# Kernel optimization log

Hardware: AMD Instinct MI355X
Metric: run time of the kernel (lower is better)

Reference implementation:

```python
import jax, jax.numpy as jnp
import numpy as np

N_NODES = 50000
N_EDGES = 1600000
DIM_IN = 64
DIM = 64
DIM_OUT = 32
N_GRAPHS = 64
DELTA = 2.5749
BN_EPS = 1e-5


def _lin(x, W, b):
    return x @ W.T + b


def _pna_conv(x, src, dst, mlp_W, mlp_b, W1, b1, W2, b2):
    # GINConv with overridden PNA aggregate: nn(x + aggr(x_j))
    msgs = x[src]                                               # [E, d]
    n = x.shape[0]
    sums = jax.ops.segment_sum(msgs, dst, num_segments=n)       # [N, d]
    maxs = jax.ops.segment_max(msgs, dst, num_segments=n)
    cnt = jax.ops.segment_sum(jnp.ones((msgs.shape[0], 1), msgs.dtype), dst,
                              num_segments=n)                   # [N, 1]
    means = sums / cnt
    var = jax.nn.relu(jax.ops.segment_sum(msgs * msgs, dst, num_segments=n) / cnt
                      - means * means)
    aggr = jnp.concatenate([sums, maxs, means, var], axis=1)    # [N, 4d]
    comb = jnp.concatenate([aggr, (cnt / DELTA) * aggr, (DELTA / cnt) * aggr],
                           axis=1)                              # [N, 12d]
    a = _lin(comb, mlp_W, mlp_b)                                # [N, d]
    h = x + a                                                   # (1+eps)*x + aggr, eps=0
    return _lin(jax.nn.relu(_lin(h, W1, b1)), W2, b2)


def _bn(x, g, b):
    # BatchNorm1d with batch statistics (training-mode stats, biased var)
    m = x.mean(axis=0)
    v = ((x - m) ** 2).mean(axis=0)
    return g * (x - m) / jnp.sqrt(v + BN_EPS) + b


def setup_inputs() -> dict:
    key = jax.random.key(0)
    ks = jax.random.split(key, 32)
    x = jax.random.normal(ks[0], (N_NODES, DIM_IN), dtype=jnp.float32)
    src = jax.random.randint(ks[1], (N_EDGES,), 0, N_NODES)
    dst = jax.random.randint(ks[2], (N_EDGES,), 0, N_NODES)
    # guarantee every node has >=1 incoming edge (original divides by bincount)
    dst = dst.at[:N_NODES].set(jnp.arange(N_NODES))
    edge_index = jnp.stack([src, dst]).astype(jnp.int32)
    batch = jnp.sort(jax.random.randint(ks[3], (N_NODES,), 0, N_GRAPHS)).astype(jnp.int32)

    def w(k, shape):
        return jax.random.normal(k, shape, dtype=jnp.float32) * 0.1

    d = {"x": x, "edge_index": edge_index, "batch": batch}
    i = 4
    for c in ("c1", "c2", "c3"):
        d[f"{c}_mlp_W"] = w(ks[i], (DIM, DIM * 12)); i += 1
        d[f"{c}_mlp_b"] = jnp.zeros((DIM,), jnp.float32)
        d[f"{c}_W1"] = w(ks[i], (DIM, DIM)); i += 1
        d[f"{c}_b1"] = jnp.zeros((DIM,), jnp.float32)
        d[f"{c}_W2"] = w(ks[i], (DIM, DIM)); i += 1
        d[f"{c}_b2"] = jnp.zeros((DIM,), jnp.float32)
    for b in ("bn1", "bn2", "bn3"):
        d[f"{b}_g"] = jnp.ones((DIM,), jnp.float32)
        d[f"{b}_b"] = jnp.zeros((DIM,), jnp.float32)
    d["fc1_W"] = w(ks[i], (DIM, DIM)); i += 1
    d["fc1_b"] = jnp.zeros((DIM,), jnp.float32)
    d["fc2_W"] = w(ks[i], (DIM_OUT, DIM)); i += 1
    d["fc2_b"] = jnp.zeros((DIM_OUT,), jnp.float32)
    return d


def reference(x, edge_index, batch,
              c1_mlp_W, c1_mlp_b, c1_W1, c1_b1, c1_W2, c1_b2, bn1_g, bn1_b,
              c2_mlp_W, c2_mlp_b, c2_W1, c2_b1, c2_W2, c2_b2, bn2_g, bn2_b,
              c3_mlp_W, c3_mlp_b, c3_W1, c3_b1, c3_W2, c3_b2, bn3_g, bn3_b,
              fc1_W, fc1_b, fc2_W, fc2_b):
    src, dst = edge_index[0], edge_index[1]
    h = jax.nn.relu(_pna_conv(x, src, dst, c1_mlp_W, c1_mlp_b, c1_W1, c1_b1, c1_W2, c1_b2))
    h = _bn(h, bn1_g, bn1_b)
    h = jax.nn.relu(_pna_conv(h, src, dst, c2_mlp_W, c2_mlp_b, c2_W1, c2_b1, c2_W2, c2_b2))
    h = _bn(h, bn2_g, bn2_b)
    h = jax.nn.relu(_pna_conv(h, src, dst, c3_mlp_W, c3_mlp_b, c3_W1, c3_b1, c3_W2, c3_b2))
    h = _bn(h, bn3_g, bn3_b)
    g = jax.ops.segment_sum(h, batch, num_segments=N_GRAPHS)   # global_add_pool
    g = jax.nn.relu(_lin(g, fc1_W, fc1_b))                     # dropout disabled (eval)
    g = _lin(g, fc2_W, fc2_b)
    return jax.nn.log_softmax(g, axis=-1)
```

## Files before the change

### kernel.cpp

```cpp
#include <hip/hip_runtime.h>

#define NN 50000
#define NE 1600000
#define DD 64
#define NGRAPH 64
#define DOUT 32
#define DELTA_F 2.5749f
#define BN_EPS_F 1e-5f

typedef unsigned short ushort;
typedef __attribute__((ext_vector_type(8))) short short8;
typedef __attribute__((ext_vector_type(4))) float floatx4;

static __device__ __forceinline__ float blo(unsigned u) {
    return __uint_as_float(u << 16);
}
static __device__ __forceinline__ float bhi(unsigned u) {
    return __uint_as_float(u & 0xFFFF0000u);
}
static __device__ __forceinline__ float bu2f(ushort u) {
    return __uint_as_float(((unsigned)u) << 16);
}
static __device__ __forceinline__ ushort f2bu(float f) {
    unsigned u = __float_as_uint(f);
    unsigned r = (u + 0x7FFF + ((u >> 16) & 1)) >> 16;
    return (ushort)r;
}
static __device__ __forceinline__ unsigned pk(float a, float b) {
    return ((unsigned)f2bu(b) << 16) | (unsigned)f2bu(a);
}

__global__ void k_prep(const float* __restrict__ x, ushort* __restrict__ XH,
                       const float* __restrict__ w0, const float* __restrict__ w1,
                       const float* __restrict__ w2,
                       const float* __restrict__ a0, const float* __restrict__ a1,
                       const float* __restrict__ a2, const float* __restrict__ a3,
                       const float* __restrict__ a4, const float* __restrict__ a5,
                       ushort* __restrict__ Wb, float* __restrict__ Wsm,
                       int* __restrict__ counts, float* __restrict__ bnstat,
                       float* __restrict__ gpool) {
    int i = blockIdx.x * 256 + threadIdx.x;
    if (i < NN) counts[i] = 0;
    if (i < 384) bnstat[i] = 0.f;
    if (i < NGRAPH * DD) gpool[i] = 0.f;
    if (i < NN * 16) {
        float4 v = *(const float4*)(x + (size_t)i * 4);
        ushort4 h;
        h.x = f2bu(v.x); h.y = f2bu(v.y); h.z = f2bu(v.z); h.w = f2bu(v.w);
        *(ushort4*)(XH + (size_t)i * 4) = h;
    }
    if (i < 3 * 65536) {
        int layer = i / 65536, r = i % 65536;
        const float* w = (layer == 0) ? w0 : ((layer == 1) ? w1 : w2);
        int c = r / 16384, r2 = r % 16384;
        int kb = r2 >> 11, r3 = r2 & 2047;
        int t = r3 >> 9, r4 = r3 & 511;
        int l = r4 >> 3, j = r4 & 7;
        int k = kb * 32 + (l >> 4) * 8 + j;
        int o = t * 16 + (l & 15);
        int g = (c == 0) ? 0 : ((c == 3) ? 2 : 1);
        float wv = w[o * 768 + g * 256 + k];
        ushort h = f2bu(wv);
        Wb[i] = (c == 2) ? f2bu(wv - bu2f(h)) : h;
    } else if (i < 3 * 65536 + 6 * 4096) {
        int r2 = i - 3 * 65536;
        int l = r2 >> 12, r = r2 & 4095;
        const float* w = (l == 0) ? a0 : (l == 1) ? a1 : (l == 2) ? a2
                       : (l == 3) ? a3 : (l == 4) ? a4 : a5;
        int o = r >> 6, j = r & 63;
        Wsm[l * 4096 + j * 64 + o] = w[r];
    }
}

__global__ void k_rank(const int* __restrict__ dst, int* __restrict__ counts,
                       int* __restrict__ rank) {
    int e = blockIdx.x * 256 + threadIdx.x;
    if (e < NE) rank[e] = atomicAdd(&counts[dst[e]], 1);
}

__global__ void k_scan_a(const int* __restrict__ counts, int* __restrict__ blockSums) {
    __shared__ int red[256];
    int tid = threadIdx.x;
    int gid = blockIdx.x * 256 + tid;
    int v = (gid < NN) ? counts[gid] : 0;
    red[tid] = v;
    __syncthreads();
    for (int s = 128; s > 0; s >>= 1) {
        if (tid < s) red[tid] += red[tid + s];
        __syncthreads();
    }
    if (tid == 0) blockSums[blockIdx.x] = red[0];
}

__global__ void k_scan_b(const int* __restrict__ blockSums, int* __restrict__ blockBase) {
    __shared__ int sh[256];
    int tid = threadIdx.x;
    int v = (tid < 196) ? blockSums[tid] : 0;
    sh[tid] = v;
    __syncthreads();
    for (int off = 1; off < 256; off <<= 1) {
        int t = (tid >= off) ? sh[tid - off] : 0;
        __syncthreads();
        sh[tid] += t;
        __syncthreads();
    }
    blockBase[tid] = sh[tid] - v;
}

__global__ void k_scan_c(const int* __restrict__ counts, const int* __restrict__ blockBase,
                         int* __restrict__ row_ptr) {
    __shared__ int sh[256];
    int tid = threadIdx.x;
    int gid = blockIdx.x * 256 + tid;
    int v = (gid < NN) ? counts[gid] : 0;
    sh[tid] = v;
    __syncthreads();
    for (int off = 1; off < 256; off <<= 1) {
        int t = (tid >= off) ? sh[tid - off] : 0;
        __syncthreads();
        sh[tid] += t;
        __syncthreads();
    }
    int excl = blockBase[blockIdx.x] + sh[tid] - v;
    if (gid <= NN) row_ptr[gid] = excl;
}

__global__ void k_place(const int* __restrict__ src, const int* __restrict__ dst,
                        const int* __restrict__ rank, const int* __restrict__ row_ptr,
                        int* __restrict__ csr_src) {
    int e = blockIdx.x * 256 + threadIdx.x;
    if (e < NE) csr_src[row_ptr[dst[e]] + rank[e]] = src[e];
}

#define MBIAS(i) aux[i]
#define B1V(i)   aux[64 + (i)]
#define B2V(i)   aux[128 + (i)]
#define DEGV(m)  aux[192 + (m)]
#define AFFS(i)  aux[224 + (i)]
#define AFFB(i)  aux[288 + (i)]

__global__ __launch_bounds__(256, 4) void k_fused(
    const ushort* __restrict__ XHin, ushort* __restrict__ XHout,
    float* __restrict__ Yf,
    const int* __restrict__ row_ptr, const int* __restrict__ csr_src,
    const ushort* __restrict__ Wbh,
    const float* __restrict__ mlp_b,
    const float* __restrict__ W1t, const float* __restrict__ b1,
    const float* __restrict__ W2t, const float* __restrict__ b2,
    const float* __restrict__ affstat, const float* __restrict__ affg,
    const float* __restrict__ affb,
    float* __restrict__ bnstat) {
    __shared__ __align__(16) char smem[27008];
    ushort* const Agh = (ushort*)smem;
    ushort* const Agl = (ushort*)(smem + 12800);
    float* const aux = (float*)(smem + 25600);
    float* const hsf = (float*)smem;

    const int tid = threadIdx.x;
    const int node0 = blockIdx.x * 32;

    if (tid < 64) {
        MBIAS(tid) = mlp_b[tid];
        B1V(tid) = b1[tid];
        B2V(tid) = b2[tid];
        float A = 1.f, Bv = 0.f;
        if (affstat) {
            float mean = affstat[tid] * (1.f / NN);
            float var = fmaxf(affstat[64 + tid] * (1.f / NN) - mean * mean, 0.f);
            float inv = rsqrtf(var + BN_EPS_F);
            A = affg[tid] * inv;
            Bv = affb[tid] - mean * A;
        }
        AFFS(tid) = A;
        AFFB(tid) = Bv;
    }
    __syncthreads();

    {
        const int l8 = tid & 7;
        const int m = tid >> 3;
        const int node = node0 + m;
        const int f0 = l8 * 8;
        const ushort* Xp = XHin + f0;

        float s[8], q[8], mx[8];
#pragma unroll
        for (int i = 0; i < 8; ++i) { s[i] = 0.f; q[i] = 0.f; mx[i] = -3.402823466e38f; }

        auto acc8 = [&](const uint4& rr) {
            float v0 = blo(rr.x), v1 = bhi(rr.x);
            float v2 = blo(rr.y), v3 = bhi(rr.y);
            float v4 = blo(rr.z), v5 = bhi(rr.z);
            float v6 = blo(rr.w), v7 = bhi(rr.w);
            s[0] += v0; q[0] = fmaf(v0, v0, q[0]); mx[0] = fmaxf(mx[0], v0);
            s[1] += v1; q[1] = fmaf(v1, v1, q[1]); mx[1] = fmaxf(mx[1], v1);
            s[2] += v2; q[2] = fmaf(v2, v2, q[2]); mx[2] = fmaxf(mx[2], v2);
            s[3] += v3; q[3] = fmaf(v3, v3, q[3]); mx[3] = fmaxf(mx[3], v3);
            s[4] += v4; q[4] = fmaf(v4, v4, q[4]); mx[4] = fmaxf(mx[4], v4);
            s[5] += v5; q[5] = fmaf(v5, v5, q[5]); mx[5] = fmaxf(mx[5], v5);
            s[6] += v6; q[6] = fmaf(v6, v6, q[6]); mx[6] = fmaxf(mx[6], v6);
            s[7] += v7; q[7] = fmaf(v7, v7, q[7]); mx[7] = fmaxf(mx[7], v7);
        };

        int beg = 0, end = 0;
        if (node < NN) { beg = row_ptr[node]; end = row_ptr[node + 1]; }
        const int deg = end - beg;
        const int nb = (deg + 3) >> 2;

        uint4 ra[4], rb[4];
        int ia[4];
        if (nb > 0) {
#pragma unroll
            for (int j = 0; j < 4; ++j) {
                int e = beg + j;
                ia[j] = csr_src[(e < end) ? e : end - 1];
            }
#pragma unroll
            for (int j = 0; j < 4; ++j)
                ra[j] = *(const uint4*)(Xp + (size_t)ia[j] * 64);
            if (nb > 1) {
#pragma unroll
                for (int j = 0; j < 4; ++j) {
                    int e = beg + 4 + j;
                    ia[j] = csr_src[(e < end) ? e : end - 1];
                }
            }
        }
        for (int t = 0; t < nb; ++t) {
            if (t + 1 < nb) {
#pragma unroll
                for (int j = 0; j < 4; ++j)
                    rb[j] = *(const uint4*)(Xp + (size_t)ia[j] * 64);
            }
            if (t + 2 < nb) {
                int b2e = beg + (t + 2) * 4;
#pragma unroll
                for (int j = 0; j < 4; ++j) {
                    int e = b2e + j;
                    ia[j] = csr_src[(e < end) ? e : end - 1];
                }
            }
            int cnt = end - (beg + t * 4);
            if (cnt >= 4) {
#pragma unroll
                for (int j = 0; j < 4; ++j) acc8(ra[j]);
            } else {
#pragma unroll
                for (int j = 0; j < 4; ++j) if (j < cnt) acc8(ra[j]);
            }
            if (t + 1 < nb) {
#pragma unroll
                for (int j = 0; j < 4; ++j) ra[j] = rb[j];
            }
        }

        float cdeg = (node < NN) ? (float)deg : 1.f;
        float rc = 1.0f / cdeg;
        float var[8];
#pragma unroll
        for (int i = 0; i < 8; ++i) {
            float mean = s[i] * rc;
            var[i] = fmaxf(q[i] * rc - mean * mean, 0.f);
            if (node >= NN) { mx[i] = 0.f; var[i] = 0.f; }
        }
#pragma unroll
        for (int i = 0; i < 8; ++i) {
            float Af = AFFS(f0 + i), Bf = AFFB(f0 + i);
            s[i] = Af * s[i] + cdeg * Bf;
            mx[i] = Af * mx[i] + Bf;
            var[i] = Af * Af * var[i];
        }
        ushort* dh = Agh + m * 200 + f0;
        ushort* dl = Agl + m * 200 + f0;
        auto emit8 = [&](const float* v, int off) {
            ushort h0 = f2bu(v[0]), h1 = f2bu(v[1]), h2 = f2bu(v[2]), h3 = f2bu(v[3]);
            ushort h4 = f2bu(v[4]), h5 = f2bu(v[5]), h6 = f2bu(v[6]), h7 = f2bu(v[7]);
            uint4 hv;
            hv.x = (unsigned)h0 | ((unsigned)h1 << 16);
            hv.y = (unsigned)h2 | ((unsigned)h3 << 16);
            hv.z = (unsigned)h4 | ((unsigned)h5 << 16);
            hv.w = (unsigned)h6 | ((unsigned)h7 << 16);
            uint4 lv;
            lv.x = pk(v[0] - bu2f(h0), v[1] - bu2f(h1));
            lv.y = pk(v[2] - bu2f(h2), v[3] - bu2f(h3));
            lv.z = pk(v[4] - bu2f(h4), v[5] - bu2f(h5));
            lv.w = pk(v[6] - bu2f(h6), v[7] - bu2f(h7));
            *(uint4*)(dh + off) = hv;
            *(uint4*)(dl + off) = lv;
        };
        emit8(s, 0);
        emit8(mx, 64);
        emit8(var, 128);
        if (l8 == 0) DEGV(m) = cdeg;
    }
    __syncthreads();

    const int ln = tid & 63, wvi = tid >> 6;
    const int quad = ln >> 4, l16 = ln & 15;
    const int mtile = wvi >> 1;
    const int nt0 = (wvi & 1) * 2;

    const ushort* ArowH = Agh + (mtile * 16 + l16) * 200 + quad * 8;
    const ushort* ArowL = Agl + (mtile * 16 + l16) * 200 + quad * 8;
    short8 afh[6], afl[6];
#pragma unroll
    for (int i = 0; i < 6; ++i) {
        const int off = (i >> 1) * 64 + (i & 1) * 32;
        afh[i] = *(const short8*)(ArowH + off);
        afl[i] = *(const short8*)(ArowL + off);
    }
    __syncthreads();

#pragma unroll
    for (int nti = 0; nti < 2; ++nti) {
        const int nt = nt0 + nti;
        floatx4 aA0 = (floatx4){0.f, 0.f, 0.f, 0.f};
        floatx4 aB0 = (floatx4){0.f, 0.f, 0.f, 0.f};
        floatx4 aA1 = (floatx4){0.f, 0.f, 0.f, 0.f};
        floatx4 aB1 = (floatx4){0.f, 0.f, 0.f, 0.f};
        floatx4 aA2 = (floatx4){0.f, 0.f, 0.f, 0.f};
        floatx4 aB2 = (floatx4){0.f, 0.f, 0.f, 0.f};
#pragma unroll
        for (int kb = 0; kb < 8; ++kb) {
            const int am = (kb < 4) ? kb : ((kb < 6) ? (kb - 4) : (kb - 2));
            const int base = ((kb * 4 + nt) * 512) + ln * 8;
            short8 w0 = *(const short8*)(Wbh + base);
            short8 w1h = *(const short8*)(Wbh + 16384 + base);
            short8 w2 = *(const short8*)(Wbh + 3 * 16384 + base);
            if (kb == 4 || kb == 5) {
                aB0 = __builtin_amdgcn_mfma_f32_16x16x32_bf16(afh[am], w0, aB0, 0, 0, 0);
                aB1 = __builtin_amdgcn_mfma_f32_16x16x32_bf16(afh[am], w1h, aB1, 0, 0, 0);
                aB2 = __builtin_amdgcn_mfma_f32_16x16x32_bf16(afh[am], w2, aB2, 0, 0, 0);
            } else {
                short8 w1l = *(const short8*)(Wbh + 2 * 16384 + base);
                aA0 = __builtin_amdgcn_mfma_f32_16x16x32_bf16(afh[am], w0, aA0, 0, 0, 0);
                aA1 = __builtin_amdgcn_mfma_f32_16x16x32_bf16(afh[am], w1h, aA1, 0, 0, 0);
                aA1 = __builtin_amdgcn_mfma_f32_16x16x32_bf16(afl[am], w1h, aA1, 0, 0, 0);
                aA1 = __builtin_amdgcn_mfma_f32_16x16x32_bf16(afh[am], w1l, aA1, 0, 0, 0);
                aA2 = __builtin_amdgcn_mfma_f32_16x16x32_bf16(afh[am], w2, aA2, 0, 0, 0);
            }
        }
#pragma unroll
        for (int r = 0; r < 4; ++r) {
            int m = mtile * 16 + quad * 4 + r;
            float dg = DEGV(m), rcd = 1.f / dg;
            float cA2 = DELTA_F * rcd;
            float cB2 = DELTA_F * rcd * rcd;
            float cA1 = dg * (1.0f / DELTA_F);
            int n = nt * 16 + l16;
            hsf[n * 34 + m] = aA0[r] + rcd * aB0[r]
                            + cA2 * aA2[r] + cB2 * aB2[r]
                            + cA1 * aA1[r] + (1.0f / DELTA_F) * aB1[r];
        }
    }
    __syncthreads();

    const int tx = tid & 15, ty = tid >> 4;
    const int o0 = tx * 4, n0 = ty * 2;
#pragma unroll
    for (int ni = 0; ni < 2; ++ni) {
        int n = n0 + ni;
        int node = node0 + n;
        float xa4[4] = {0.f, 0.f, 0.f, 0.f};
        if (node < NN) {
            ushort4 hx = *(const ushort4*)(XHin + (size_t)node * DD + o0);
            xa4[0] = AFFS(o0 + 0) * bu2f(hx.x) + AFFB(o0 + 0);
            xa4[1] = AFFS(o0 + 1) * bu2f(hx.y) + AFFB(o0 + 1);
            xa4[2] = AFFS(o0 + 2) * bu2f(hx.z) + AFFB(o0 + 2);
            xa4[3] = AFFS(o0 + 3) * bu2f(hx.w) + AFFB(o0 + 3);
        }
#pragma unroll
        for (int oi = 0; oi < 4; ++oi) {
            int idx = (o0 + oi) * 34 + n;
            hsf[idx] = hsf[idx] + xa4[oi] + MBIAS(o0 + oi);
        }
    }
    __syncthreads();

    const float2* const hs2 = (const float2*)hsf;
    float l1[8];
#pragma unroll
    for (int i = 0; i < 8; ++i) l1[i] = 0.f;
#pragma unroll 4
    for (int j = 0; j < 64; ++j) {
        float2 a = hs2[j * 17 + ty];
        const float4 wv4 = *(const float4*)(W1t + j * 64 + o0);
        l1[0] += a.x * wv4.x; l1[1] += a.x * wv4.y; l1[2] += a.x * wv4.z; l1[3] += a.x * wv4.w;
        l1[4] += a.y * wv4.x; l1[5] += a.y * wv4.y; l1[6] += a.y * wv4.z; l1[7] += a.y * wv4.w;
    }
    __syncthreads();
#pragma unroll
    for (int ni = 0; ni < 2; ++ni)
#pragma unroll
        for (int oi = 0; oi < 4; ++oi)
            hsf[(o0 + oi) * 34 + n0 + ni] = fmaxf(l1[ni * 4 + oi] + B1V(o0 + oi), 0.f);
    __syncthreads();

    float l2[8];
#pragma unroll
    for (int i = 0; i < 8; ++i) l2[i] = 0.f;
#pragma unroll 4
    for (int j = 0; j < 64; ++j) {
        float2 a = hs2[j * 17 + ty];
        const float4 wv4 = *(const float4*)(W2t + j * 64 + o0);
        l2[0] += a.x * wv4.x; l2[1] += a.x * wv4.y; l2[2] += a.x * wv4.z; l2[3] += a.x * wv4.w;
        l2[4] += a.y * wv4.x; l2[5] += a.y * wv4.y; l2[6] += a.y * wv4.z; l2[7] += a.y * wv4.w;
    }
    __syncthreads();
#pragma unroll
    for (int ni = 0; ni < 2; ++ni) {
        int node = node0 + n0 + ni;
        float4 yv;
        yv.x = fmaxf(l2[ni * 4 + 0] + B2V(o0 + 0), 0.f);
        yv.y = fmaxf(l2[ni * 4 + 1] + B2V(o0 + 1), 0.f);
        yv.z = fmaxf(l2[ni * 4 + 2] + B2V(o0 + 2), 0.f);
        yv.w = fmaxf(l2[ni * 4 + 3] + B2V(o0 + 3), 0.f);
        if (node < NN) {
            if (XHout) {
                ushort4 h;
                h.x = f2bu(yv.x); h.y = f2bu(yv.y);
                h.z = f2bu(yv.z); h.w = f2bu(yv.w);
                *(ushort4*)(XHout + (size_t)node * DD + o0) = h;
            }
            if (Yf) *(float4*)(Yf + (size_t)node * DD + o0) = yv;
        }
        hsf[(o0 + 0) * 34 + n0 + ni] = yv.x;
        hsf[(o0 + 1) * 34 + n0 + ni] = yv.y;
        hsf[(o0 + 2) * 34 + n0 + ni] = yv.z;
        hsf[(o0 + 3) * 34 + n0 + ni] = yv.w;
    }
    __syncthreads();

    if (tid < 64) {
        float s = 0.f, sq = 0.f;
        int lim = NN - node0;
        if (lim > 32) lim = 32;
        for (int n = 0; n < lim; ++n) {
            float v = hsf[tid * 34 + n];
            s += v;
            sq += v * v;
        }
        atomicAdd(&bnstat[tid], s);
        atomicAdd(&bnstat[64 + tid], sq);
    }
}

__global__ __launch_bounds__(256) void k_pool(
    const float* __restrict__ Y, const float* __restrict__ bs,
    const float* __restrict__ g, const float* __restrict__ b,
    const int* __restrict__ batch, float* __restrict__ gpool) {
    __shared__ float sc[64], shf[64], pool[512];
    int tid = threadIdx.x;
    if (tid < 64) {
        float mean = bs[tid] * (1.f / NN);
        float var = fmaxf(bs[64 + tid] * (1.f / NN) - mean * mean, 0.f);
        float inv = rsqrtf(var + BN_EPS_F);
        float s = g[tid] * inv;
        sc[tid] = s;
        shf[tid] = b[tid] - mean * s;
    }
    __syncthreads();
    int i = blockIdx.x * 256 + tid;
    int n = i >> 4, fq = (i & 15) * 4;
    float4 r = make_float4(0.f, 0.f, 0.f, 0.f);
    bool valid = i < NN * 16;
    if (valid) {
        float4 y = *(const float4*)(Y + (size_t)i * 4);
        r.x = y.x * sc[fq + 0] + shf[fq + 0];
        r.y = y.y * sc[fq + 1] + shf[fq + 1];
        r.z = y.z * sc[fq + 2] + shf[fq + 2];
        r.w = y.w * sc[fq + 3] + shf[fq + 3];
    }
    int nfirst = blockIdx.x * 16;
    int nlast = nfirst + 15;
    if (nlast >= NN) nlast = NN - 1;
    int gmin = batch[nfirst], gmax = batch[nlast];
    int span = gmax - gmin + 1;
    if (span <= 8) {
        for (int j = tid; j < span * 64; j += 256) pool[j] = 0.f;
        __syncthreads();
        if (valid) {
            int gb = batch[n] - gmin;
            atomicAdd(&pool[gb * 64 + fq + 0], r.x);
            atomicAdd(&pool[gb * 64 + fq + 1], r.y);
            atomicAdd(&pool[gb * 64 + fq + 2], r.z);
            atomicAdd(&pool[gb * 64 + fq + 3], r.w);
        }
        __syncthreads();
        for (int j = tid; j < span * 64; j += 256)
            atomicAdd(&gpool[(size_t)(gmin + (j >> 6)) * 64 + (j & 63)], pool[j]);
    } else {
        if (valid) {
            float* gp = gpool + (size_t)batch[n] * DD + fq;
            atomicAdd(gp + 0, r.x);
            atomicAdd(gp + 1, r.y);
            atomicAdd(gp + 2, r.z);
            atomicAdd(gp + 3, r.w);
        }
    }
}

__global__ __launch_bounds__(256) void k_head(const float* __restrict__ gpool,
                                              const float* __restrict__ fc1W, const float* __restrict__ fc1b,
                                              const float* __restrict__ fc2W, const float* __restrict__ fc2b,
                                              float* __restrict__ out) {
    __shared__ float sh[12576];
    float* const gs = sh;
    float* const w1t = sh + 4096;
    float* const z1s = sh + 8256;
    float* const b1s = sh + 12416;
    float* const b2s = sh + 12480;
    float* const w2t = sh;
    float* const z2s = sh + 4096;

    int tid = threadIdx.x;
    for (int i = tid; i < 4096; i += 256) {
        gs[i] = gpool[i];
        int o = i >> 6, j = i & 63;
        w1t[j * 65 + o] = fc1W[i];
    }
    if (tid < 64) b1s[tid] = fc1b[tid];
    if (tid < 32) b2s[tid] = fc2b[tid];
    __syncthreads();
    {
        int tx = tid & 15, ty = tid >> 4, o0 = tx * 4, g0 = ty * 4;
        float acc[16];
#pragma unroll
        for (int i = 0; i < 16; ++i) acc[i] = 0.f;
        for (int j = 0; j < 64; ++j) {
            float w0 = w1t[j * 65 + o0 + 0], w1 = w1t[j * 65 + o0 + 1];
            float w2 = w1t[j * 65 + o0 + 2], w3 = w1t[j * 65 + o0 + 3];
#pragma unroll
            for (int gi = 0; gi < 4; ++gi) {
                float a = gs[(g0 + gi) * 64 + j];
                acc[gi * 4 + 0] += a * w0; acc[gi * 4 + 1] += a * w1;
                acc[gi * 4 + 2] += a * w2; acc[gi * 4 + 3] += a * w3;
            }
        }
        __syncthreads();
#pragma unroll
        for (int gi = 0; gi < 4; ++gi)
#pragma unroll
            for (int oi = 0; oi < 4; ++oi)
                z1s[(g0 + gi) * 65 + o0 + oi] = fmaxf(acc[gi * 4 + oi] + b1s[o0 + oi], 0.f);
    }
    for (int i = tid; i < 2048; i += 256) {
        int o = i >> 6, j = i & 63;
        w2t[j * 33 + o] = fc2W[i];
    }
    __syncthreads();
    {
        int tx = tid & 7, ty = tid >> 3, o0 = tx * 4, g0 = ty * 2;
        float acc[8];
#pragma unroll
        for (int i = 0; i < 8; ++i) acc[i] = 0.f;
        for (int j = 0; j < 64; ++j) {
            float w0 = w2t[j * 33 + o0 + 0], w1 = w2t[j * 33 + o0 + 1];
            float w2 = w2t[j * 33 + o0 + 2], w3 = w2t[j * 33 + o0 + 3];
            float a0 = z1s[(g0 + 0) * 65 + j];
            float a1 = z1s[(g0 + 1) * 65 + j];
            acc[0] += a0 * w0; acc[1] += a0 * w1; acc[2] += a0 * w2; acc[3] += a0 * w3;
            acc[4] += a1 * w0; acc[5] += a1 * w1; acc[6] += a1 * w2; acc[7] += a1 * w3;
        }
#pragma unroll
        for (int gi = 0; gi < 2; ++gi)
#pragma unroll
            for (int oi = 0; oi < 4; ++oi)
                z2s[(g0 + gi) * 33 + o0 + oi] = acc[gi * 4 + oi] + b2s[o0 + oi];
    }
    __syncthreads();
    if (tid < 64) {
        float m = -3.402823466e38f;
        for (int c = 0; c < DOUT; ++c) m = fmaxf(m, z2s[tid * 33 + c]);
        float s = 0.f;
        for (int c = 0; c < DOUT; ++c) s += expf(z2s[tid * 33 + c] - m);
        float lse = m + logf(s);
        for (int c = 0; c < DOUT; ++c)
            out[tid * DOUT + c] = z2s[tid * 33 + c] - lse;
    }
}

extern "C" void kernel_launch(void* const* d_in, const int* in_sizes, int n_in,
                              void* d_out, int out_size, void* d_ws, size_t ws_size,
                              hipStream_t stream) {
    const float* x = (const float*)d_in[0];
    const int* ei = (const int*)d_in[1];
    const int* src = ei;
    const int* dst = ei + NE;
    const int* batch = (const int*)d_in[2];
    const float *mlpW[3], *mlpB[3], *w1[3], *bb1[3], *w2[3], *bb2[3], *bng[3], *bnb[3];
    for (int l = 0; l < 3; ++l) {
        mlpW[l] = (const float*)d_in[3 + 6 * l];
        mlpB[l] = (const float*)d_in[4 + 6 * l];
        w1[l]   = (const float*)d_in[5 + 6 * l];
        bb1[l]  = (const float*)d_in[6 + 6 * l];
        w2[l]   = (const float*)d_in[7 + 6 * l];
        bb2[l]  = (const float*)d_in[8 + 6 * l];
        bng[l]  = (const float*)d_in[21 + 2 * l];
        bnb[l]  = (const float*)d_in[22 + 2 * l];
    }
    const float* fc1W = (const float*)d_in[27];
    const float* fc1b = (const float*)d_in[28];
    const float* fc2W = (const float*)d_in[29];
    const float* fc2b = (const float*)d_in[30];
    float* out = (float*)d_out;

    char* ws = (char*)d_ws;
    size_t off = 0;
    auto alloc = [&](size_t bytes) -> void* {
        void* p = ws + off;
        off = (off + bytes + 511) & ~(size_t)511;
        return p;
    };
    int* counts    = (int*)alloc((size_t)NN * 4);
    int* row_ptr   = (int*)alloc((size_t)(NN + 1) * 4);
    int* rank      = (int*)alloc((size_t)NE * 4);
    int* blockSums = (int*)alloc(256 * 4);
    int* blockBase = (int*)alloc(256 * 4);
    int* csr_src   = (int*)alloc((size_t)NE * 4);
    float* Yb      = (float*)alloc((size_t)NN * DD * 4);
    ushort* XHA    = (ushort*)alloc((size_t)NN * DD * 2);
    ushort* XHB    = (ushort*)alloc((size_t)NN * DD * 2);
    ushort* Wb     = (ushort*)alloc((size_t)3 * 65536 * 2);
    float* Wsm     = (float*)alloc((size_t)6 * 4096 * 4);
    float* bnstat  = (float*)alloc(384 * 4);
    float* gpool   = (float*)alloc((size_t)NGRAPH * DD * 4);
    (void)ws_size; (void)in_sizes; (void)n_in; (void)out_size;

    k_prep<<<3125, 256, 0, stream>>>(x, XHA,
                                     mlpW[0], mlpW[1], mlpW[2],
                                     w1[0], w2[0], w1[1], w2[1], w1[2], w2[2],
                                     Wb, Wsm, counts, bnstat, gpool);
    k_rank<<<6250, 256, 0, stream>>>(dst, counts, rank);
    k_scan_a<<<196, 256, 0, stream>>>(counts, blockSums);
    k_scan_b<<<1, 256, 0, stream>>>(blockSums, blockBase);
    k_scan_c<<<196, 256, 0, stream>>>(counts, blockBase, row_ptr);
    k_place<<<6250, 256, 0, stream>>>(src, dst, rank, row_ptr, csr_src);

    k_fused<<<1563, 256, 0, stream>>>(XHA, XHB, nullptr, row_ptr, csr_src,
                                      Wb, mlpB[0],
                                      Wsm, bb1[0], Wsm + 4096, bb2[0],
                                      nullptr, nullptr, nullptr,
                                      bnstat);
    k_fused<<<1563, 256, 0, stream>>>(XHB, XHA, nullptr, row_ptr, csr_src,
                                      Wb + 65536, mlpB[1],
                                      Wsm + 2 * 4096, bb1[1], Wsm + 3 * 4096, bb2[1],
                                      bnstat, bng[0], bnb[0],
                                      bnstat + 128);
    k_fused<<<1563, 256, 0, stream>>>(XHA, nullptr, Yb, row_ptr, csr_src,
                                      Wb + 2 * 65536, mlpB[2],
                                      Wsm + 4 * 4096, bb1[2], Wsm + 5 * 4096, bb2[2],
                                      bnstat + 128, bng[1], bnb[1],
                                      bnstat + 256);
    k_pool<<<3125, 256, 0, stream>>>(Yb, bnstat + 256, bng[2], bnb[2], batch, gpool);
    k_head<<<1, 256, 0, stream>>>(gpool, fc1W, fc1b, fc2W, fc2b, out);
}
```

Measured before the change: 498.8 us.

## Fuse global add pool into last conv layer and drop the rank array

The final batch-norm affine is folded algebraically into the head: pooled sums of pre-BN activations are scaled, and the shift is multiplied by a per-graph node count. That count is built with atomics in the count kernel. Pooling now happens inside the third fused conv kernel using the per-block smem tile, which removes the fp32 Y buffer write and the separate pool kernel. Separately, CSR placement now decrements counts atomically instead of storing a per-edge rank array, which saves a 6.4MB write and read but makes the order of edges within each row nondeterministic.

```diff
diff --git a/kernel.cpp b/kernel.cpp
--- a/kernel.cpp
+++ b/kernel.cpp
@@ -38,11 +38,12 @@
                        const float* __restrict__ a4, const float* __restrict__ a5,
                        ushort* __restrict__ Wb, float* __restrict__ Wsm,
                        int* __restrict__ counts, float* __restrict__ bnstat,
-                       float* __restrict__ gpool) {
+                       float* __restrict__ gpool, int* __restrict__ gcnt) {
     int i = blockIdx.x * 256 + threadIdx.x;
     if (i < NN) counts[i] = 0;
     if (i < 384) bnstat[i] = 0.f;
     if (i < NGRAPH * DD) gpool[i] = 0.f;
+    if (i < NGRAPH) gcnt[i] = 0;
     if (i < NN * 16) {
         float4 v = *(const float4*)(x + (size_t)i * 4);
         ushort4 h;
@@ -72,10 +73,11 @@
     }
 }
 
-__global__ void k_rank(const int* __restrict__ dst, int* __restrict__ counts,
-                       int* __restrict__ rank) {
+__global__ void k_count(const int* __restrict__ dst, int* __restrict__ counts,
+                        const int* __restrict__ batch, int* __restrict__ gcnt) {
     int e = blockIdx.x * 256 + threadIdx.x;
-    if (e < NE) rank[e] = atomicAdd(&counts[dst[e]], 1);
+    if (e < NE) atomicAdd(&counts[dst[e]], 1);
+    if (e < NN) atomicAdd(&gcnt[batch[e]], 1);
 }
 
 __global__ void k_scan_a(const int* __restrict__ counts, int* __restrict__ blockSums) {
@@ -126,10 +128,14 @@
 }
 
 __global__ void k_place(const int* __restrict__ src, const int* __restrict__ dst,
-                        const int* __restrict__ rank, const int* __restrict__ row_ptr,
+                        int* __restrict__ counts, const int* __restrict__ row_ptr,
                         int* __restrict__ csr_src) {
     int e = blockIdx.x * 256 + threadIdx.x;
-    if (e < NE) csr_src[row_ptr[dst[e]] + rank[e]] = src[e];
+    if (e < NE) {
+        int d = dst[e];
+        int r = atomicAdd(&counts[d], -1) - 1;
+        csr_src[row_ptr[d] + r] = src[e];
+    }
 }
 
 #define MBIAS(i) aux[i]
@@ -141,7 +147,6 @@
 
 __global__ __launch_bounds__(256, 4) void k_fused(
     const ushort* __restrict__ XHin, ushort* __restrict__ XHout,
-    float* __restrict__ Yf,
     const int* __restrict__ row_ptr, const int* __restrict__ csr_src,
     const ushort* __restrict__ Wbh,
     const float* __restrict__ mlp_b,
@@ -149,11 +154,13 @@
     const float* __restrict__ W2t, const float* __restrict__ b2,
     const float* __restrict__ affstat, const float* __restrict__ affg,
     const float* __restrict__ affb,
-    float* __restrict__ bnstat) {
-    __shared__ __align__(16) char smem[27008];
+    float* __restrict__ bnstat,
+    const int* __restrict__ batch, float* __restrict__ gpool, int do_pool) {
+    __shared__ __align__(16) char smem[27136];
     ushort* const Agh = (ushort*)smem;
     ushort* const Agl = (ushort*)(smem + 12800);
     float* const aux = (float*)(smem + 25600);
+    int* const ibatch = (int*)(smem + 27008);
     float* const hsf = (float*)smem;
 
     const int tid = threadIdx.x;
@@ -173,6 +180,10 @@
         }
         AFFS(tid) = A;
         AFFB(tid) = Bv;
+    }
+    if (tid < 32) {
+        int node = node0 + tid;
+        ibatch[tid] = (do_pool && node < NN) ? batch[node] : -1;
     }
     __syncthreads();
 
@@ -415,14 +426,11 @@
         yv.y = fmaxf(l2[ni * 4 + 1] + B2V(o0 + 1), 0.f);
         yv.z = fmaxf(l2[ni * 4 + 2] + B2V(o0 + 2), 0.f);
         yv.w = fmaxf(l2[ni * 4 + 3] + B2V(o0 + 3), 0.f);
-        if (node < NN) {
-            if (XHout) {
-                ushort4 h;
-                h.x = f2bu(yv.x); h.y = f2bu(yv.y);
-                h.z = f2bu(yv.z); h.w = f2bu(yv.w);
-                *(ushort4*)(XHout + (size_t)node * DD + o0) = h;
-            }
-            if (Yf) *(float4*)(Yf + (size_t)node * DD + o0) = yv;
+        if (node < NN && XHout) {
+            ushort4 h;
+            h.x = f2bu(yv.x); h.y = f2bu(yv.y);
+            h.z = f2bu(yv.z); h.w = f2bu(yv.w);
+            *(ushort4*)(XHout + (size_t)node * DD + o0) = h;
         }
         hsf[(o0 + 0) * 34 + n0 + ni] = yv.x;
         hsf[(o0 + 1) * 34 + n0 + ni] = yv.y;
@@ -433,90 +441,63 @@
 
     if (tid < 64) {
         float s = 0.f, sq = 0.f;
+        float pacc = 0.f;
+        int curg = ibatch[0];
         int lim = NN - node0;
         if (lim > 32) lim = 32;
         for (int n = 0; n < lim; ++n) {
             float v = hsf[tid * 34 + n];
             s += v;
             sq += v * v;
-        }
+            if (do_pool) {
+                int g = ibatch[n];
+                if (g != curg) {
+                    atomicAdd(&gpool[(size_t)curg * DD + tid], pacc);
+                    pacc = 0.f;
+                    curg = g;
+                }
+                pacc += v;
+            }
+        }
+        if (do_pool && curg >= 0)
+            atomicAdd(&gpool[(size_t)curg * DD + tid], pacc);
         atomicAdd(&bnstat[tid], s);
         atomicAdd(&bnstat[64 + tid], sq);
     }
 }
 
-__global__ __launch_bounds__(256) void k_pool(
-    const float* __restrict__ Y, const float* __restrict__ bs,
-    const float* __restrict__ g, const float* __restrict__ b,
-    const int* __restrict__ batch, float* __restrict__ gpool) {
-    __shared__ float sc[64], shf[64], pool[512];
-    int tid = threadIdx.x;
-    if (tid < 64) {
-        float mean = bs[tid] * (1.f / NN);
-        float var = fmaxf(bs[64 + tid] * (1.f / NN) - mean * mean, 0.f);
-        float inv = rsqrtf(var + BN_EPS_F);
-        float s = g[tid] * inv;
-        sc[tid] = s;
-        shf[tid] = b[tid] - mean * s;
-    }
-    __syncthreads();
-    int i = blockIdx.x * 256 + tid;
-    int n = i >> 4, fq = (i & 15) * 4;
-    float4 r = make_float4(0.f, 0.f, 0.f, 0.f);
-    bool valid = i < NN * 16;
-    if (valid) {
-        float4 y = *(const float4*)(Y + (size_t)i * 4);
-        r.x = y.x * sc[fq + 0] + shf[fq + 0];
-        r.y = y.y * sc[fq + 1] + shf[fq + 1];
-        r.z = y.z * sc[fq + 2] + shf[fq + 2];
-        r.w = y.w * sc[fq + 3] + shf[fq + 3];
-    }
-    int nfirst = blockIdx.x * 16;
-    int nlast = nfirst + 15;
-    if (nlast >= NN) nlast = NN - 1;
-    int gmin = batch[nfirst], gmax = batch[nlast];
-    int span = gmax - gmin + 1;
-    if (span <= 8) {
-        for (int j = tid; j < span * 64; j += 256) pool[j] = 0.f;
-        __syncthreads();
-        if (valid) {
-            int gb = batch[n] - gmin;
-            atomicAdd(&pool[gb * 64 + fq + 0], r.x);
-            atomicAdd(&pool[gb * 64 + fq + 1], r.y);
-            atomicAdd(&pool[gb * 64 + fq + 2], r.z);
-            atomicAdd(&pool[gb * 64 + fq + 3], r.w);
-        }
-        __syncthreads();
-        for (int j = tid; j < span * 64; j += 256)
-            atomicAdd(&gpool[(size_t)(gmin + (j >> 6)) * 64 + (j & 63)], pool[j]);
-    } else {
-        if (valid) {
-            float* gp = gpool + (size_t)batch[n] * DD + fq;
-            atomicAdd(gp + 0, r.x);
-            atomicAdd(gp + 1, r.y);
-            atomicAdd(gp + 2, r.z);
-            atomicAdd(gp + 3, r.w);
-        }
-    }
-}
-
 __global__ __launch_bounds__(256) void k_head(const float* __restrict__ gpool,
+                                              const float* __restrict__ bs3,
+                                              const float* __restrict__ g3,
+                                              const float* __restrict__ b3,
+                                              const int* __restrict__ gcnt,
                                               const float* __restrict__ fc1W, const float* __restrict__ fc1b,
                                               const float* __restrict__ fc2W, const float* __restrict__ fc2b,
                                               float* __restrict__ out) {
-    __shared__ float sh[12576];
+    __shared__ float sh[12640];
     float* const gs = sh;
     float* const w1t = sh + 4096;
     float* const z1s = sh + 8256;
     float* const b1s = sh + 12416;
     float* const b2s = sh + 12480;
+    float* const sc3 = sh + 12512;
+    float* const shf3 = sh + 12576;
     float* const w2t = sh;
     float* const z2s = sh + 4096;
 
     int tid = threadIdx.x;
+    if (tid < 64) {
+        float mean = bs3[tid] * (1.f / NN);
+        float var = fmaxf(bs3[64 + tid] * (1.f / NN) - mean * mean, 0.f);
+        float inv = rsqrtf(var + BN_EPS_F);
+        float A = g3[tid] * inv;
+        sc3[tid] = A;
+        shf3[tid] = b3[tid] - mean * A;
+    }
+    __syncthreads();
     for (int i = tid; i < 4096; i += 256) {
-        gs[i] = gpool[i];
         int o = i >> 6, j = i & 63;
+        gs[i] = sc3[j] * gpool[i] + shf3[j] * (float)gcnt[o];
         w1t[j * 65 + o] = fc1W[i];
     }
     if (tid < 64) b1s[tid] = fc1b[tid];
@@ -614,44 +595,43 @@
     };
     int* counts    = (int*)alloc((size_t)NN * 4);
     int* row_ptr   = (int*)alloc((size_t)(NN + 1) * 4);
-    int* rank      = (int*)alloc((size_t)NE * 4);
     int* blockSums = (int*)alloc(256 * 4);
     int* blockBase = (int*)alloc(256 * 4);
     int* csr_src   = (int*)alloc((size_t)NE * 4);
-    float* Yb      = (float*)alloc((size_t)NN * DD * 4);
     ushort* XHA    = (ushort*)alloc((size_t)NN * DD * 2);
     ushort* XHB    = (ushort*)alloc((size_t)NN * DD * 2);
     ushort* Wb     = (ushort*)alloc((size_t)3 * 65536 * 2);
     float* Wsm     = (float*)alloc((size_t)6 * 4096 * 4);
     float* bnstat  = (float*)alloc(384 * 4);
     float* gpool   = (float*)alloc((size_t)NGRAPH * DD * 4);
+    int* gcnt      = (int*)alloc(NGRAPH * 4);
     (void)ws_size; (void)in_sizes; (void)n_in; (void)out_size;
 
     k_prep<<<3125, 256, 0, stream>>>(x, XHA,
                                      mlpW[0], mlpW[1], mlpW[2],
                                      w1[0], w2[0], w1[1], w2[1], w1[2], w2[2],
-                                     Wb, Wsm, counts, bnstat, gpool);
-    k_rank<<<6250, 256, 0, stream>>>(dst, counts, rank);
+                                     Wb, Wsm, counts, bnstat, gpool, gcnt);
+    k_count<<<6250, 256, 0, stream>>>(dst, counts, batch, gcnt);
     k_scan_a<<<196, 256, 0, stream>>>(counts, blockSums);
     k_scan_b<<<1, 256, 0, stream>>>(blockSums, blockBase);
     k_scan_c<<<196, 256, 0, stream>>>(counts, blockBase, row_ptr);
-    k_place<<<6250, 256, 0, stream>>>(src, dst, rank, row_ptr, csr_src);
-
-    k_fused<<<1563, 256, 0, stream>>>(XHA, XHB, nullptr, row_ptr, csr_src,
+    k_place<<<6250, 256, 0, stream>>>(src, dst, counts, row_ptr, csr_src);
+
+    k_fused<<<1563, 256, 0, stream>>>(XHA, XHB, row_ptr, csr_src,
                                       Wb, mlpB[0],
                                       Wsm, bb1[0], Wsm + 4096, bb2[0],
                                       nullptr, nullptr, nullptr,
-                                      bnstat);
-    k_fused<<<1563, 256, 0, stream>>>(XHB, XHA, nullptr, row_ptr, csr_src,
+                                      bnstat, batch, gpool, 0);
+    k_fused<<<1563, 256, 0, stream>>>(XHB, XHA, row_ptr, csr_src,
                                       Wb + 65536, mlpB[1],
                                       Wsm + 2 * 4096, bb1[1], Wsm + 3 * 4096, bb2[1],
                                       bnstat, bng[0], bnb[0],
-                                      bnstat + 128);
-    k_fused<<<1563, 256, 0, stream>>>(XHA, nullptr, Yb, row_ptr, csr_src,
+                                      bnstat + 128, batch, gpool, 0);
+    k_fused<<<1563, 256, 0, stream>>>(XHA, nullptr, row_ptr, csr_src,
                                       Wb + 2 * 65536, mlpB[2],
                                       Wsm + 4 * 4096, bb1[2], Wsm + 5 * 4096, bb2[2],
                                       bnstat + 128, bng[1], bnb[1],
-                                      bnstat + 256);
-    k_pool<<<3125, 256, 0, stream>>>(Yb, bnstat + 256, bng[2], bnb[2], batch, gpool);
-    k_head<<<1, 256, 0, stream>>>(gpool, fc1W, fc1b, fc2W, fc2b, out);
-}
+                                      bnstat + 256, batch, gpool, 1);
+    k_head<<<1, 256, 0, stream>>>(gpool, bnstat + 256, bng[2], bnb[2], gcnt,
+                                  fc1W, fc1b, fc2W, fc2b, out);
+}
```

Result: slower. 808.0 us (+62.0%).
